# Optimization experiments

Measured on AMD Instinct MI355X. Metric: run time of the kernel, lower is better.

## Reference

```python
import jax, jax.numpy as jnp
import numpy as np
from jax.scipy.special import gammaln

# ---- constants matching init_kwargs ----
D = 64            # num_nodes
K = 64            # DiBS latent rank (k = d default)
P = 32            # n_particles
N_MC = 16         # MC graph samples for score-function grad estimator
PROJ = 128        # proj_dims
N = 2048          # observations
H = 5.0           # h_latent (Frobenius squared-exponential kernel bandwidth)
ALPHA = 0.2       # alpha_linear * t  (single SVGD step)
STEP = 0.005      # SVGD step size
ALPHA_MU = 1.0
ALPHA_LAMBD = float(D + 2)
THETA_MU = 0.0
P_EDGE = 4.0 / (D - 1)          # Erdos-Renyi edge prob (~2 expected edges/node)
LATENT_STD = 1.0 / np.sqrt(K)   # DiBS default latent prior std


def bge_log_marginal(g, data, mu0, alpha_mu, alpha_lambd):
    """BGe log marginal likelihood log p(data | G) for 0/1 adjacency g [d,d]."""
    n, d = data.shape
    small_t = alpha_mu * (alpha_lambd - d - 1.0) / (alpha_mu + 1.0)
    xbar = data.mean(0)
    xc = data - xbar
    R = small_t * jnp.eye(d) + xc.T @ xc \
        + (n * alpha_mu / (n + alpha_mu)) * jnp.outer(xbar - mu0, xbar - mu0)

    def masked_slogdet(mask):  # logdet of R restricted to mask-selected rows/cols
        m = jnp.outer(mask, mask)
        return jnp.linalg.slogdet(m * R + (1.0 - m) * jnp.eye(d))[1]

    def node_score(j):
        parents = g[:, j].astype(R.dtype)
        pj = jnp.maximum(parents, (jnp.arange(d) == j).astype(R.dtype))
        l = jnp.sum(parents)
        log_gamma = (0.5 * (jnp.log(alpha_mu) - jnp.log(n + alpha_mu))
                     + gammaln(0.5 * (n + alpha_lambd - d + l + 1.0))
                     - gammaln(0.5 * (alpha_lambd - d + l + 1.0))
                     - 0.5 * n * jnp.log(jnp.pi)
                     + 0.5 * (alpha_lambd - d + 2.0 * l + 1.0) * jnp.log(small_t))
        return (log_gamma
                + 0.5 * (n + alpha_lambd - d + l) * masked_slogdet(parents)
                - 0.5 * (n + alpha_lambd - d + l + 1.0) * masked_slogdet(pj))

    return jnp.sum(jax.vmap(node_score)(jnp.arange(d)))


def _dense(key, fan_in, fan_out):
    return jax.random.normal(key, (fan_in, fan_out), jnp.float32) * 0.05


def setup_inputs() -> dict:
    key = jax.random.key(0)
    ks = jax.random.split(key, 16)
    return {
        "z_gt": jax.random.normal(ks[0], (N, D), jnp.float32),
        "init_particles_z": jax.random.normal(ks[1], (P, D, K, 2), jnp.float32) * LATENT_STD,
        "enc_w0": _dense(ks[2], D * D, 20), "enc_b0": jnp.zeros(20, jnp.float32),
        "enc_w1": _dense(ks[3], 20, D),     "enc_b1": jnp.zeros(D, jnp.float32),
        "enc_w2": _dense(ks[4], D, D),      "enc_b2": jnp.zeros(D, jnp.float32),
        "mu_w0": _dense(ks[5], D, D), "mu_b0": jnp.zeros(D, jnp.float32),
        "mu_w1": _dense(ks[6], D, D), "mu_b1": jnp.zeros(D, jnp.float32),
        "lv_w0": _dense(ks[7], D, D), "lv_b0": jnp.zeros(D, jnp.float32),
        "lv_w1": _dense(ks[8], D, D), "lv_b1": jnp.zeros(D, jnp.float32),
        "dec_w0": _dense(ks[9], D, 10),       "dec_b0": jnp.zeros(10, jnp.float32),
        "dec_w1": _dense(ks[10], 10, PROJ),   "dec_b1": jnp.zeros(PROJ, jnp.float32),
        "dec_w2": _dense(ks[11], PROJ, PROJ), "dec_b2": jnp.zeros(PROJ, jnp.float32),
        "seed": 0,
    }


def reference(z_gt, init_particles_z, enc_w0, enc_b0, enc_w1, enc_b1, enc_w2, enc_b2,
              mu_w0, mu_b0, mu_w1, mu_b1, lv_w0, lv_b0, lv_w1, lv_b1,
              dec_w0, dec_b0, dec_w1, dec_b1, dec_w2, dec_b2, seed):
    key = jax.random.key(seed)
    d = z_gt.shape[1]
    od = 1.0 - jnp.eye(d)
    z = init_particles_z                                   # [P,d,k,2]
    u, v = z[..., 0], z[..., 1]
    scores = jnp.einsum('pik,pjk->pij', u, v)              # [P,d,d]
    probs = jax.nn.sigmoid(ALPHA * scores) * od            # soft graph, zero diag

    # --- score-function estimate of grad_z log E_G[p(data|G)] (DiBS marginal) ---
    key, sk = jax.random.split(key)
    gs = jax.random.bernoulli(sk, probs[:, None], (P, N_MC, d, d)).astype(z.dtype) * od
    mu0_inf = jnp.zeros(d, z.dtype)
    logp = jax.vmap(jax.vmap(
        lambda g: bge_log_marginal(g, z_gt, mu0_inf, 1.0, d + 2.0)))(gs)   # [P,S]
    w = jax.nn.softmax(logp, axis=1)                       # self-normalized weights
    M = ALPHA * (gs - probs[:, None]) * od                 # d log q(G|Z) / d scores
    grad_u = jnp.einsum('ps,psij,pjk->pik', w, M, v)
    grad_v = jnp.einsum('ps,psij,pik->pjk', w, M, u)

    # --- grad of soft-graph ER prior + Gaussian latent prior ---
    logit_pe = jnp.log(P_EDGE) - jnp.log1p(-P_EDGE)
    Mp = ALPHA * probs * (1.0 - probs) * logit_pe * od
    grad_u = grad_u + jnp.einsum('pij,pjk->pik', Mp, v) - u / (LATENT_STD ** 2)
    grad_v = grad_v + jnp.einsum('pij,pik->pjk', Mp, u) - v / (LATENT_STD ** 2)
    grads = jnp.stack([grad_u, grad_v], axis=-1)           # [P,d,k,2]

    # --- one SVGD step with Frobenius squared-exponential kernel ---
    zf = z.reshape(P, -1)
    gf = grads.reshape(P, -1)
    sq = jnp.sum((zf[:, None] - zf[None]) ** 2, -1)
    Kmat = jnp.exp(-sq / H)                                # symmetric [P,P]
    rep = (-2.0 / H) * (Kmat @ zf - zf * Kmat.sum(1, keepdims=True))
    z_new = z + STEP * ((Kmat @ gf + rep) / P).reshape(z.shape)

    # --- hard graphs: particle_to_g_lim (alpha -> inf) ---
    s2 = jnp.einsum('pik,pjk->pij', z_new[..., 0], z_new[..., 1])
    g_hard = (s2 > 0).astype(z.dtype) * od                 # [P,d,d]

    mu0_bge = jnp.full(d, THETA_MU, z.dtype)
    log_p_z_given_g = jax.vmap(
        lambda g: bge_log_marginal(g, z_gt, mu0_bge, ALPHA_MU, ALPHA_LAMBD))(g_hard)

    # --- q(z | G) encoder (batched over particles) ---
    gf2 = g_hard.reshape(g_hard.shape[0], d * d)
    h = jax.nn.relu(gf2 @ enc_w0 + enc_b0)
    h = jax.nn.relu(h @ enc_w1 + enc_b1)
    h = jax.nn.relu(h @ enc_w2 + enc_b2)
    q_mu = jax.nn.relu(h @ mu_w0 + mu_b0) @ mu_w1 + mu_b1
    q_lv = jax.nn.relu(h @ lv_w0 + lv_b0) @ lv_w1 + lv_b1

    key, rk = jax.random.split(key)
    eps = jax.random.normal(rk, q_lv.shape, q_lv.dtype)
    q_z = q_mu + eps * jnp.exp(0.5 * q_lv)                 # reparameterize

    # --- decoder ---
    hdec = jax.nn.relu(q_z @ dec_w0 + dec_b0)
    hdec = jax.nn.relu(hdec @ dec_w1 + dec_b1)
    recons = hdec @ dec_w2 + dec_b2                        # [P, PROJ]

    return recons, log_p_z_given_g, q_z, q_mu, q_lv, g_hard, z_new
```

## Files before the change

### kernel.cpp

```cpp
#include <hip/hip_runtime.h>
#include <stdint.h>
#include <math.h>

typedef unsigned long long u64;
typedef unsigned int u32;
typedef unsigned short u16;

#define C_P 32
#define C_S 16
#define C_D 64
#define C_N 2048

#define R_OFF      0
#define CTAB_OFF   4160
#define KEYS_OFF   4224
#define PROBS_OFF  4232
#define GROW_OFF   135304
#define GCOL_OFF   168072
#define NS_OFF     200840
#define W_OFF      233608
#define GF_OFF     234120
#define KM_OFF     365192
#define ZN_OFF     365704
#define NS2_OFF    496776

#define WL_LIST0 16

#define HBLK 768
#define TB3 1728
#define TB2 2208
#define TB1 2208
#define TB0 1920
#define E3 (HBLK + TB3)
#define E2 (E3 + TB2)
#define E1 (E2 + TB1)
#define NBLK_ALL (E1 + TB0)

#define O_REC   0
#define O_LOGP  4096
#define O_QZ    4128
#define O_QMU   6176
#define O_QLV   8224
#define O_GH    10272
#define O_ZN    141344
#define O_TOTAL 403488

__device__ __forceinline__ void tf2x32(u32 k0, u32 k1, u32 x0, u32 x1,
                                       u32& o0, u32& o1) {
  u32 ks2 = k0 ^ k1 ^ 0x1BD11BDAu;
  x0 += k0; x1 += k1;
#define TFR(r) { x0 += x1; x1 = (x1 << r) | (x1 >> (32 - r)); x1 ^= x0; }
  TFR(13) TFR(15) TFR(26) TFR(6)   x0 += k1;  x1 += ks2 + 1u;
  TFR(17) TFR(29) TFR(16) TFR(24)  x0 += ks2; x1 += k0 + 2u;
  TFR(13) TFR(15) TFR(26) TFR(6)   x0 += k0;  x1 += k1 + 3u;
  TFR(17) TFR(29) TFR(16) TFR(24)  x0 += k1;  x1 += ks2 + 4u;
  TFR(13) TFR(15) TFR(26) TFR(6)   x0 += ks2; x1 += k0 + 5u;
#undef TFR
  o0 = x0; o1 = x1;
}

__device__ __forceinline__ double d_erfinv(double x) {
  double w = -log1p(-x * x);
  double p;
  if (w < 5.0) {
    w -= 2.5;
    p = 2.81022636e-08;
    p = 3.43273939e-07  + p * w;
    p = -3.5233877e-06  + p * w;
    p = -4.39150654e-06 + p * w;
    p = 0.00021858087   + p * w;
    p = -0.00125372503  + p * w;
    p = -0.00417768164  + p * w;
    p = 0.246640727     + p * w;
    p = 1.50140941      + p * w;
  } else {
    w = sqrt(w) - 3.0;
    p = -0.000200214257;
    p = 0.000100950558  + p * w;
    p = 0.00134934322   + p * w;
    p = -0.00367342844  + p * w;
    p = 0.00573950773   + p * w;
    p = -0.0076224613   + p * w;
    p = 0.00943887047   + p * w;
    p = 1.00167406      + p * w;
    p = 2.83297682      + p * w;
  }
  return p * x;
}

__device__ __forceinline__ double stirl(double z) {
  double zi = 1.0 / z;
  double zi2 = zi * zi;
  double s = (z - 0.5) * log(z) - z + 0.9189385332046727;
  s += zi * (1.0 / 12.0 - zi2 * (1.0 / 360.0 - zi2 * (1.0 / 1260.0)));
  return s;
}

__global__ void k_R(const float* x, double* ws, const int* seedp) {
  __shared__ double pS[8][64], pX[8][64];
  __shared__ double xbar[64];
  int j = blockIdx.x, t = threadIdx.x;
  int i = t & 63, c = t >> 6;
  if (j == 0) {
    if (t < 64) {
      int l = t;
      double term = (l >= 2) ? log((2049.0 + (double)l) / (4.0 * (1.0 + (double)l)))
                             : 0.0;
      double v = term;
#pragma unroll
      for (int off = 2; off <= 32; off <<= 1) {
        double o = __shfl_up(v, off, 64);
        if (l >= off) v += o;
      }
      const double LOG_HALF = -0.6931471805599453;
      double c0 = -0.5 * log(2049.0)
                - 1024.0 * log(3.14159265358979323846);
      double seed = (l & 1)
        ? c0 + stirl(1026.0) + 2.5 * LOG_HALF
        : c0 + stirl(1025.5) + 0.12078223763524522235 + 1.5 * LOG_HALF;
      ws[CTAB_OFF + l] = seed + v;
    }
    if (t < 8) ((u32*)(ws + GF_OFF))[t] = 0;
    if (t == 0) {
      u32 kk0 = 0u, kk1 = (u32)seedp[0];
      u32 a0, a1, s0, s1, r0, r1, d0, d1;
      tf2x32(kk0, kk1, 0u, 0u, a0, a1);
      tf2x32(kk0, kk1, 0u, 1u, s0, s1);
      tf2x32(a0, a1, 0u, 0u, d0, d1); (void)d0; (void)d1;
      tf2x32(a0, a1, 0u, 1u, r0, r1);
      u32* keys = (u32*)(ws + KEYS_OFF);
      keys[0] = s0; keys[1] = s1; keys[2] = r0; keys[3] = r1;
    }
  }
  double sx = 0.0, sxx = 0.0;
  for (int n = c * 256; n < (c + 1) * 256; n++) {
    double xi = (double)x[n * 64 + i];
    double xj = (double)x[n * 64 + j];
    sx += xi; sxx += xi * xj;
  }
  pS[c][i] = sx; pX[c][i] = sxx;
  __syncthreads();
  if (t < 64) {
    double S = 0.0, X = 0.0;
    for (int cc = 0; cc < 8; cc++) { S += pS[cc][i]; X += pX[cc][i]; }
    xbar[i] = S / 2048.0;
    pX[0][i] = X;
  }
  __syncthreads();
  if (t < 64) {
    double xbi = xbar[i], xbj = xbar[j];
    double s = pX[0][i] - 2048.0 * xbi * xbj + (2048.0 / 2049.0) * xbi * xbj;
    if (i == j) s += 0.5;
    ((float*)(ws + R_OFF))[i * 64 + j] = (float)s;
  }
}

__global__ __launch_bounds__(64) void k_probs(const float* z, double* ws) {
  float* probs = (float*)(ws + PROBS_OFF);
  int b = blockIdx.x; int p = b >> 6, i = b & 63;
  int j = threadIdx.x;
  __shared__ float V[64 * 65];
  __shared__ float us[64];
  int k = j;
  us[k] = z[((p * 64 + i) * 64 + k) * 2 + 0];
  for (int jj = 0; jj < 64; jj++)
    V[jj * 65 + k] = z[((p * 64 + jj) * 64 + k) * 2 + 1];
  __syncthreads();
  float s = 0.f;
  for (int kk = 0; kk < 64; kk++)
    s += us[kk] * V[j * 65 + kk];
  float pr = (i == j) ? 0.f : 1.f / (1.f + expf(-0.2f * s));
  probs[(p * 64 + i) * 64 + j] = pr;
}

__global__ void k_sample(double* ws) {
  const float* probs = (const float*)(ws + PROBS_OFF);
  const u32* keys = (const u32*)(ws + KEYS_OFF);
  u64* grow = (u64*)(ws + GROW_OFF);
  u64* gcol = (u64*)(ws + GCOL_OFF);
  u32* wl = (u32*)(ws + GF_OFF);
  int ps = blockIdx.x;
  int p = ps >> 4;
  int j = threadIdx.x;
  u32 k0 = keys[0], k1 = keys[1];
  u64 colmask = 0;
  for (int i = 0; i < 64; i++) {
    u32 lin = (u32)(ps * 4096 + i * 64 + j);
    u32 o0, o1; tf2x32(k0, k1, 0u, lin, o0, o1);
    u32 bits = o0 ^ o1;
    float f = __uint_as_float((bits >> 9) | 0x3f800000u) - 1.0f;
    bool bit = (f < probs[(p * 64 + i) * 64 + j]);
    u64 rm = __ballot(bit);
    if (j == 0) grow[ps * 64 + i] = rm;
    if (bit) colmask |= (1ull << i);
  }
  gcol[ps * 64 + j] = colmask;
  int m = (int)__popcll(colmask) + 1;
  int tier = (m <= 29) ? 0 : (m <= 32) ? 1 : (m <= 35) ? 2 : (m <= 40) ? 3 : 4;
#pragma unroll
  for (int t = 0; t < 5; t++) {
    u64 b = __ballot(tier == t);
    if (tier == t) {
      int leader = (int)__builtin_ctzll(b);
      u32 off = (u32)__popcll(b & ((1ull << j) - 1ull));
      u32 base = 0;
      if (j == leader) base = atomicAdd(&wl[t], (u32)__popcll(b));
      base = (u32)__shfl((int)base, leader, 64);
      wl[WL_LIST0 + t * 32768 + base + off] = (u32)(ps * 64 + j);
    }
  }
}

__device__ __forceinline__ float rdlane(float x, int l) {
  return __uint_as_float(__builtin_amdgcn_readlane(__float_as_uint(x), (u32)l));
}

template<int MMAX>
__device__ __forceinline__ void tier_body(const float* Rf, const double* ctab,
                                          const u64* masks, double* nodescore,
                                          const u32* wl, int tier,
                                          u32 brel, u32 nb, int (*idx)[64]) {
  int w = threadIdx.x >> 6;
  int lane = threadIdx.x & 63;
  u32 cnt = wl[tier];
  const u32* list = wl + WL_LIST0 + tier * 32768;
  for (u32 ti = brel * 4 + (u32)w; ti < cnt; ti += nb * 4) {
    int task = (int)list[ti];
    int j = task & 63;
    u64 mask = masks[task];
    int P = (int)__popcll(mask);
    int m = P + 1;
    idx[w][lane] = 0;
    __builtin_amdgcn_wave_barrier();
    u64 below = mask & ((1ull << lane) - 1ull);
    if ((mask >> lane) & 1ull) idx[w][(int)__popcll(below)] = lane;
    if (lane == 0) idx[w][P] = j;
    __builtin_amdgcn_wave_barrier();
    int myrow = idx[w][lane];
    float v[MMAX];
#pragma unroll
    for (int c = 0; c < MMAX; c++)
      v[c] = Rf[idx[w][c] * 64 + myrow];
    float mypiv = 1.0f;
#pragma unroll
    for (int k = 0; k < MMAX; k++) {
      if (k < m) {
        float dk = rdlane(v[k], k);
        if (lane == k) mypiv = dk;
        float ns = -v[k] * __builtin_amdgcn_rcpf(dk);
#pragma unroll
        for (int b = k + 1; b < MMAX; b++)
          v[b] += ns * rdlane(v[k], b);
      }
    }
    float lastd = __shfl(mypiv, P, 64);
    float lv = (lane < m) ? __logf(mypiv) : 0.f;
    for (int off = 32; off > 0; off >>= 1) lv += __shfl_down(lv, off, 64);
    if (lane == 0) {
      double l = (double)P;
      nodescore[task] = ctab[P]
                      - 0.5 * (2050.0 + l) * (double)__logf(lastd)
                      - 0.5 * (double)lv;
    }
    __builtin_amdgcn_wave_barrier();
  }
}

#define WB() __builtin_amdgcn_wave_barrier()

__device__ void heavy_body(const float* Rf, const double* ctab,
                           const u64* masks, double* nodescore,
                           const u32* wl, u32 brel, u32 nb,
                           float* T, int* idx) {
  if (threadIdx.x >= 64) return;
  int lane = threadIdx.x;
  u32 cnt = wl[4];
  const u32* list = wl + WL_LIST0 + 4 * 32768;
  for (u32 ii = brel; ii < cnt; ii += nb) {
    WB();
    int task = (int)list[ii];
    int j = task & 63;
    u64 mask = masks[task];
    int P = (int)__popcll(mask);
    int m = P + 1;
    u64 below = mask & ((1ull << lane) - 1ull);
    if ((mask >> lane) & 1ull) idx[(int)__popcll(below)] = lane;
    if (lane == 0) idx[P] = j;
    WB();
    int trLane = (lane * (lane + 1)) >> 1;
    if (lane < m) {
      int cidx = idx[lane];
      int tr = 0;
      for (int r = 0; r < m; r++) {
        if (lane <= r) T[tr + lane] = Rf[idx[r] * 64 + cidx];
        tr += r + 1;
      }
    }
    WB();
    float mypiv = 1.0f, lastd = 1.0f;
    float v[40];
#pragma unroll
    for (int c = 0; c < 40; c++)
      v[c] = T[trLane + c];
#pragma unroll
    for (int k = 0; k < 40; k++) {
      if (k < m) {
        float dk = rdlane(v[k], k);
        if (lane == k) mypiv = dk;
        lastd = dk;
        float ns = -v[k] * __builtin_amdgcn_rcpf(dk);
#pragma unroll
        for (int b = k + 1; b < 40; b++)
          v[b] += ns * rdlane(v[k], b);
      }
    }
    if (m > 40) {
      for (int b = 40; b < m; b++) {
        float acc = 0.f;
#pragma unroll
        for (int k = 0; k < 40; k++) {
          float dk = rdlane(v[k], k);
          float abk = rdlane(v[k], b);
          acc += v[k] * abk * __builtin_amdgcn_rcpf(dk);
        }
        if (lane >= b) T[trLane + b] -= acc;
      }
      WB();
      for (int k = 40; k < m; k++) {
        float dk = T[((k * (k + 1)) >> 1) + k];
        if (lane == k) mypiv = dk;
        lastd = dk;
        float sk = T[trLane + k] * __builtin_amdgcn_rcpf(dk);
        for (int b = k + 1; b < m; b++) {
          float abk = T[((b * (b + 1)) >> 1) + k];
          if (lane >= b) T[trLane + b] -= sk * abk;
        }
        WB();
      }
    }
    double vv = (lane < m) ? log((double)mypiv) : 0.0;
    for (int off = 32; off > 0; off >>= 1) vv += __shfl_down(vv, off, 64);
    if (lane == 0) {
      double logB = vv;
      double logA = logB - log((double)lastd);
      double l = (double)P;
      nodescore[task] = ctab[P]
                      + 0.5 * (2050.0 + l) * logA
                      - 0.5 * (2051.0 + l) * logB;
    }
  }
}

__global__ __launch_bounds__(256) void k_chol_all(const float* Rf, const double* ctab,
                                                  const u64* masks, double* nodescore,
                                                  const u32* wl) {
  __shared__ int idx4[4][64];
  __shared__ float T[2080];
  __shared__ int idxh[64];
  u32 b = blockIdx.x;
  if (b < HBLK)    heavy_body(Rf, ctab, masks, nodescore, wl, b, HBLK, T, idxh);
  else if (b < E3) tier_body<40>(Rf, ctab, masks, nodescore, wl, 3, b - HBLK, TB3, idx4);
  else if (b < E2) tier_body<35>(Rf, ctab, masks, nodescore, wl, 2, b - E3, TB2, idx4);
  else if (b < E1) tier_body<32>(Rf, ctab, masks, nodescore, wl, 1, b - E2, TB1, idx4);
  else             tier_body<29>(Rf, ctab, masks, nodescore, wl, 0, b - E1, TB0, idx4);
}

template<bool TRANSPOSE>
__global__ __launch_bounds__(64) void k_chol(const float* Rf, const double* ctab,
                                             const u64* masks, double* nodescore) {
  __shared__ float T[2080];
  __shared__ int idx[64];
  int task = blockIdx.x;
  int j = task & 63;
  int lane = threadIdx.x;
  u64 mask;
  if (TRANSPOSE) {
    int p = task >> 6;
    u64 rm = masks[p * 64 + lane];
    mask = __ballot((rm >> j) & 1ull);
  } else {
    mask = masks[task];
  }
  int P = (int)__popcll(mask);
  int m = P + 1;
  u64 below = mask & ((1ull << lane) - 1ull);
  if ((mask >> lane) & 1ull) idx[(int)__popcll(below)] = lane;
  if (lane == 0) idx[P] = j;
  __syncthreads();
  int trLane = (lane * (lane + 1)) >> 1;
  if (lane < m) {
    int cidx = idx[lane];
    int tr = 0;
    for (int r = 0; r < m; r++) {
      if (lane <= r) T[tr + lane] = Rf[idx[r] * 64 + cidx];
      tr += r + 1;
    }
  }
  __syncthreads();
  float mypiv = 1.0f, lastd = 1.0f;
  float v[40];
#pragma unroll
  for (int c = 0; c < 40; c++)
    v[c] = T[trLane + c];
#pragma unroll
  for (int k = 0; k < 40; k++) {
    if (k < m) {
      float dk = rdlane(v[k], k);
      if (lane == k) mypiv = dk;
      lastd = dk;
      float ns = -v[k] * __builtin_amdgcn_rcpf(dk);
#pragma unroll
      for (int b = k + 1; b < 40; b++)
        v[b] += ns * rdlane(v[k], b);
    }
  }
  if (m > 40) {
    for (int b = 40; b < m; b++) {
      float acc = 0.f;
#pragma unroll
      for (int k = 0; k < 40; k++) {
        float dk = rdlane(v[k], k);
        float abk = rdlane(v[k], b);
        acc += v[k] * abk * __builtin_amdgcn_rcpf(dk);
      }
      if (lane >= b) T[trLane + b] -= acc;
    }
    __syncthreads();
    for (int k = 40; k < m; k++) {
      float dk = T[((k * (k + 1)) >> 1) + k];
      if (lane == k) mypiv = dk;
      lastd = dk;
      float sk = T[trLane + k] * __builtin_amdgcn_rcpf(dk);
      for (int b = k + 1; b < m; b++) {
        float abk = T[((b * (b + 1)) >> 1) + k];
        if (lane >= b) T[trLane + b] -= sk * abk;
      }
      __syncthreads();
    }
  }
  double vv = (lane < m) ? log((double)mypiv) : 0.0;
  for (int off = 32; off > 0; off >>= 1) vv += __shfl_down(vv, off, 64);
  if (lane == 0) {
    double logB = vv;
    double logA = logB - log((double)lastd);
    double l = (double)P;
    nodescore[task] = ctab[P]
                    + 0.5 * (2050.0 + l) * logA
                    - 0.5 * (2051.0 + l) * logB;
  }
}

__global__ void k_logpw(const double* ns, double* w) {
  int p = blockIdx.x, t = threadIdx.x;
  __shared__ double part[64];
  int s = t & 15, c = t >> 4;
  double acc = 0.0;
  for (int j = c * 16; j < (c + 1) * 16; j++)
    acc += ns[(p * 16 + s) * 64 + j];
  part[t] = acc;
  __syncthreads();
  if (t < 16) part[t] = part[t] + part[t + 16] + part[t + 32] + part[t + 48];
  __syncthreads();
  if (t == 0) {
    double m = part[0];
    for (int s2 = 1; s2 < 16; s2++) m = fmax(m, part[s2]);
    double e[16], sum = 0.0;
    for (int s2 = 0; s2 < 16; s2++) { e[s2] = exp(part[s2] - m); sum += e[s2]; }
    for (int s2 = 0; s2 < 16; s2++) w[p * 16 + s2] = e[s2] / sum;
  }
}

__global__ void k_grad(double* ws, const float* z) {
  const float* probs = (const float*)(ws + PROBS_OFF);
  const double* w = ws + W_OFF;
  const u64* grow = (const u64*)(ws + GROW_OFF);
  const u64* gcol = (const u64*)(ws + GCOL_OFF);
  float* gf = (float*)(ws + GF_OFF);
  const float LOGIT = -2.6903717578966254f;
  int bb = blockIdx.x;
  int k = threadIdx.x;
  __shared__ float acc[64];
  if (bb < 2048) {
    int p = bb >> 6, i = bb & 63;
    float gb = 0.f, wsum = 0.f;
    for (int s = 0; s < 16; s++) {
      float wv = (float)w[p * 16 + s];
      wsum += wv;
      gb += wv * (float)((grow[(p * 16 + s) * 64 + i] >> k) & 1ull);
    }
    float pr = probs[(p * 64 + i) * 64 + k];
    float od = (i == k) ? 0.f : 1.f;
    acc[k] = (0.2f * (gb - pr * wsum) + 0.2f * pr * (1.f - pr) * LOGIT) * od;
    __syncthreads();
    float s = 0.f;
    for (int j = 0; j < 64; j++)
      s += acc[j] * z[((p * 64 + j) * 64 + k) * 2 + 1];
    s -= 64.f * z[((p * 64 + i) * 64 + k) * 2 + 0];
    gf[p * 8192 + (i * 64 + k) * 2 + 0] = s;
  } else if (bb < 4096) {
    int b = bb - 2048;
    int p = b >> 6, j = b & 63;
    float gb = 0.f, wsum = 0.f;
    for (int s = 0; s < 16; s++) {
      float wv = (float)w[p * 16 + s];
      wsum += wv;
      gb += wv * (float)((gcol[(p * 16 + s) * 64 + j] >> k) & 1ull);
    }
    float pr = probs[(p * 64 + k) * 64 + j];
    float od = (k == j) ? 0.f : 1.f;
    acc[k] = (0.2f * (gb - pr * wsum) + 0.2f * pr * (1.f - pr) * LOGIT) * od;
    __syncthreads();
    float s = 0.f;
    for (int i = 0; i < 64; i++)
      s += acc[i] * z[((p * 64 + i) * 64 + k) * 2 + 0];
    s -= 64.f * z[((p * 64 + j) * 64 + k) * 2 + 1];
    gf[p * 8192 + (j * 64 + k) * 2 + 1] = s;
  } else {
    float* Km = (float*)(ws + KM_OFF);
    int b = bb - 4096;
    int a = b >> 5, b2 = b & 31;
    float accf = 0.f;
    for (int d0 = k; d0 < 8192; d0 += 64) {
      float diff = z[a * 8192 + d0] - z[b2 * 8192 + d0];
      accf += diff * diff;
    }
    for (int off = 32; off > 0; off >>= 1) accf += __shfl_down(accf, off, 64);
    if (k == 0) Km[a * 32 + b2] = expf(-accf / 5.0f);
  }
}

__global__ void k_znew(const float* z, double* ws, float* out) {
  const float* Km = (const float*)(ws + KM_OFF);
  const float* gf = (const float*)(ws + GF_OFF);
  float* zn = (float*)(ws + ZN_OFF);
  int gid = blockIdx.x * 64 + threadIdx.x;
  int p = gid >> 13, t = gid & 8191;
  float zp = z[p * 8192 + t];
  float accg = 0.f, accz = 0.f, ks = 0.f;
  for (int b = 0; b < 32; b++) {
    float kv = Km[p * 32 + b];
    accg += kv * gf[b * 8192 + t];
    accz += kv * z[b * 8192 + t];
    ks += kv;
  }
  float rep = -0.4f * (accz - zp * ks);
  float v = zp + 0.005f * ((accg + rep) / 32.f);
  zn[p * 8192 + t] = v;
  out[O_ZN + p * 8192 + t] = v;
}

__global__ __launch_bounds__(64) void k_s2col(double* ws, float* out) {
  const float* zn = (const float*)(ws + ZN_OFF);
  u64* grow2 = (u64*)(ws + NS_OFF);
  int b = blockIdx.x; int p = b >> 6, i = b & 63;
  int j = threadIdx.x;
  __shared__ float V[64 * 65];
  __shared__ float us[64];
  int k = j;
  us[k] = zn[p * 8192 + (i * 64 + k) * 2 + 0];
  for (int jj = 0; jj < 64; jj++)
    V[jj * 65 + k] = zn[p * 8192 + (jj * 64 + k) * 2 + 1];
  __syncthreads();
  float s = 0.f;
  for (int kk = 0; kk < 64; kk++)
    s += us[kk] * V[j * 65 + kk];
  bool bit = (i != j) && (s > 0.0f);
  out[O_GH + (p * 64 + i) * 64 + j] = bit ? 1.0f : 0.0f;
  u64 m = __ballot(bit);
  if (j == 0) grow2[p * 64 + i] = m;
}

__global__ __launch_bounds__(256) void k_mlp(double* ws, float* out, const double* ns2,
    const float* ew0, const float* eb0, const float* ew1, const float* eb1,
    const float* ew2, const float* eb2,
    const float* mw0, const float* mb0, const float* mw1, const float* mb1,
    const float* lw0, const float* lb0, const float* lw1, const float* lb1,
    const float* dw0, const float* db0, const float* dw1, const float* db1,
    const float* dw2, const float* db2) {
  int p = blockIdx.x, t = threadIdx.x;
  int w = t >> 6, lane = t & 63;
  const u64* grow2 = (const u64*)(ws + NS_OFF);
  const u32* keys = (const u32*)(ws + KEYS_OFF);
  __shared__ float pt[4][64];
  __shared__ float e0p[4][20];
  __shared__ float h0[20], h1[64], h2[64], hm[64], hl[64];
  __shared__ float qmu[64], qlv[64], qz[64], h3[10], h4[128];

  if (w == 0) {
    double vv = ns2[p * 64 + lane];
    for (int off = 32; off > 0; off >>= 1) vv += __shfl_down(vv, off, 64);
    if (lane == 0) out[O_LOGP + p] = (float)vv;
  }

  {
    int i = t >> 2;
    int jb = (t & 3) * 16;
    u32 m16 = (u32)((grow2[p * 64 + i] >> jb) & 0xFFFFull);
    float acc[20];
#pragma unroll
    for (int o = 0; o < 20; o++) acc[o] = 0.f;
    const float4* wb = (const float4*)(ew0 + (size_t)(t * 16) * 20);
#pragma unroll
    for (int q = 0; q < 16; q++) {
      float mq = (float)((m16 >> q) & 1u);
      float4 r0 = wb[q * 5 + 0], r1 = wb[q * 5 + 1], r2 = wb[q * 5 + 2];
      float4 r3 = wb[q * 5 + 3], r4 = wb[q * 5 + 4];
      acc[0]  += mq * r0.x; acc[1]  += mq * r0.y; acc[2]  += mq * r0.z; acc[3]  += mq * r0.w;
      acc[4]  += mq * r1.x; acc[5]  += mq * r1.y; acc[6]  += mq * r1.z; acc[7]  += mq * r1.w;
      acc[8]  += mq * r2.x; acc[9]  += mq * r2.y; acc[10] += mq * r2.z; acc[11] += mq * r2.w;
      acc[12] += mq * r3.x; acc[13] += mq * r3.y; acc[14] += mq * r3.z; acc[15] += mq * r3.w;
      acc[16] += mq * r4.x; acc[17] += mq * r4.y; acc[18] += mq * r4.z; acc[19] += mq * r4.w;
    }
#pragma unroll
    for (int o = 0; o < 20; o++) {
      float v = acc[o];
      for (int off = 32; off > 0; off >>= 1) v += __shfl_down(v, off, 64);
      if (lane == 0) e0p[w][o] = v;
    }
  }
  __syncthreads();
  if (t < 20)
    h0[t] = fmaxf(eb0[t] + e0p[0][t] + e0p[1][t] + e0p[2][t] + e0p[3][t], 0.f);
  __syncthreads();

  {
    float s = 0.f;
#pragma unroll
    for (int q = 0; q < 5; q++) s += h0[w * 5 + q] * ew1[(w * 5 + q) * 64 + lane];
    pt[w][lane] = s;
  }
  __syncthreads();
  if (w == 0)
    h1[lane] = fmaxf(eb1[lane] + pt[0][lane] + pt[1][lane] + pt[2][lane] + pt[3][lane], 0.f);
  __syncthreads();

  {
    float s = 0.f;
#pragma unroll
    for (int q = 0; q < 16; q++) s += h1[w * 16 + q] * ew2[(w * 16 + q) * 64 + lane];
    pt[w][lane] = s;
  }
  __syncthreads();
  if (w == 0)
    h2[lane] = fmaxf(eb2[lane] + pt[0][lane] + pt[1][lane] + pt[2][lane] + pt[3][lane], 0.f);
  __syncthreads();

  {
    const float* W = (w < 2) ? mw0 : lw0;
    int qb = (w & 1) * 32;
    float s = 0.f;
#pragma unroll
    for (int q = 0; q < 32; q++) s += h2[qb + q] * W[(qb + q) * 64 + lane];
    pt[w][lane] = s;
  }
  __syncthreads();
  if (w == 0) hm[lane] = fmaxf(mb0[lane] + pt[0][lane] + pt[1][lane], 0.f);
  if (w == 1) hl[lane] = fmaxf(lb0[lane] + pt[2][lane] + pt[3][lane], 0.f);
  __syncthreads();

  {
    const float* W = (w < 2) ? mw1 : lw1;
    const float* src = (w < 2) ? hm : hl;
    int qb = (w & 1) * 32;
    float s = 0.f;
#pragma unroll
    for (int q = 0; q < 32; q++) s += src[qb + q] * W[(qb + q) * 64 + lane];
    pt[w][lane] = s;
  }
  __syncthreads();
  if (w == 0) qmu[lane] = mb1[lane] + pt[0][lane] + pt[1][lane];
  if (w == 1) qlv[lane] = lb1[lane] + pt[2][lane] + pt[3][lane];
  __syncthreads();

  if (w == 0) {
    u32 o0, o1;
    tf2x32(keys[2], keys[3], 0u, (u32)(p * 64 + lane), o0, o1);
    u32 bits = o0 ^ o1;
    float f = __uint_as_float((bits >> 9) | 0x3f800000u) - 1.0f;
    float LOF = __uint_as_float(0xBF7FFFFFu);
    float uu = fmaxf(LOF, f * 2.0f + LOF);
    float eps = (float)(1.4142135623730951 * d_erfinv((double)uu));
    float qzv = qmu[lane] + eps * expf(0.5f * qlv[lane]);
    qz[lane] = qzv;
    out[O_QZ  + p * 64 + lane] = qzv;
    out[O_QMU + p * 64 + lane] = qmu[lane];
    out[O_QLV + p * 64 + lane] = qlv[lane];
  }
  __syncthreads();

  {
    float s = 0.f;
    if (lane < 10) {
#pragma unroll
      for (int q = 0; q < 16; q++) s += qz[w * 16 + q] * dw0[(w * 16 + q) * 10 + lane];
    }
    pt[w][lane] = s;
  }
  __syncthreads();
  if (w == 0 && lane < 10)
    h3[lane] = fmaxf(db0[lane] + pt[0][lane] + pt[1][lane] + pt[2][lane] + pt[3][lane], 0.f);
  __syncthreads();

  {
    int o = (w >> 1) * 64 + lane;
    int qb = (w & 1) * 5;
    float s = 0.f;
#pragma unroll
    for (int q = 0; q < 5; q++) s += h3[qb + q] * dw1[(qb + q) * 128 + o];
    pt[w][lane] = s;
  }
  __syncthreads();
  if (w == 0) h4[lane]      = fmaxf(db1[lane]      + pt[0][lane] + pt[1][lane], 0.f);
  if (w == 1) h4[64 + lane] = fmaxf(db1[64 + lane] + pt[2][lane] + pt[3][lane], 0.f);
  __syncthreads();

  {
    int o = (w >> 1) * 64 + lane;
    int qb = (w & 1) * 64;
    float s = 0.f;
#pragma unroll
    for (int q = 0; q < 64; q++) s += h4[qb + q] * dw2[(qb + q) * 128 + o];
    pt[w][lane] = s;
  }
  __syncthreads();
  if (w == 0) out[O_REC + p * 128 + lane]      = db2[lane]      + pt[0][lane] + pt[1][lane];
  if (w == 1) out[O_REC + p * 128 + 64 + lane] = db2[64 + lane] + pt[2][lane] + pt[3][lane];
}

extern "C" void kernel_launch(void* const* d_in, const int* in_sizes, int n_in,
                              void* d_out, int out_size, void* d_ws, size_t ws_size,
                              hipStream_t stream) {
  (void)in_sizes; (void)n_in; (void)out_size; (void)ws_size;
  const float* z_gt = (const float*)d_in[0];
  const float* z0   = (const float*)d_in[1];
  const float* ew0 = (const float*)d_in[2];  const float* eb0 = (const float*)d_in[3];
  const float* ew1 = (const float*)d_in[4];  const float* eb1 = (const float*)d_in[5];
  const float* ew2 = (const float*)d_in[6];  const float* eb2 = (const float*)d_in[7];
  const float* mw0 = (const float*)d_in[8];  const float* mb0 = (const float*)d_in[9];
  const float* mw1 = (const float*)d_in[10]; const float* mb1 = (const float*)d_in[11];
  const float* lw0 = (const float*)d_in[12]; const float* lb0 = (const float*)d_in[13];
  const float* lw1 = (const float*)d_in[14]; const float* lb1 = (const float*)d_in[15];
  const float* dw0 = (const float*)d_in[16]; const float* db0 = (const float*)d_in[17];
  const float* dw1 = (const float*)d_in[18]; const float* db1 = (const float*)d_in[19];
  const float* dw2 = (const float*)d_in[20]; const float* db2 = (const float*)d_in[21];
  const int* seed = (const int*)d_in[22];
  double* ws = (double*)d_ws;
  float* out = (float*)d_out;
  const float* Rf = (const float*)(ws + R_OFF);
  const u32* wl = (const u32*)(ws + GF_OFF);

  k_R<<<64, 512, 0, stream>>>(z_gt, ws, seed);
  k_probs<<<C_P * C_D, 64, 0, stream>>>(z0, ws);
  k_sample<<<C_P * C_S, 64, 0, stream>>>(ws);
  k_chol_all<<<NBLK_ALL, 256, 0, stream>>>(Rf, ws + CTAB_OFF,
      (const u64*)(ws + GCOL_OFF), ws + NS_OFF, wl);
  k_logpw<<<C_P, 64, 0, stream>>>(ws + NS_OFF, ws + W_OFF);
  k_grad<<<2 * C_P * C_D + C_P * C_P, 64, 0, stream>>>(ws, z0);
  k_znew<<<(C_P * 8192) / 64, 64, 0, stream>>>(z0, ws, out);
  k_s2col<<<C_P * C_D, 64, 0, stream>>>(ws, out);
  k_chol<true><<<C_P * C_D, 64, 0, stream>>>(Rf, ws + CTAB_OFF,
      (const u64*)(ws + NS_OFF), ws + NS2_OFF);
  k_mlp<<<C_P, 256, 0, stream>>>(ws, out, ws + NS2_OFF,
      ew0, eb0, ew1, eb1, ew2, eb2,
      mw0, mb0, mw1, mb1, lw0, lb0, lw1, lb1,
      dw0, db0, dw1, db1, dw2, db2);
}
```

Baseline: 350.3 us.

## Pack two small Cholesky tasks per wavefront using half-wave bpermute

Tiers 0 and 1 (masked submatrix size up to 32) are merged into one packed path where each 64-lane wavefront handles two node-score tasks, 32 lanes each. Cross-lane pivot broadcasts use ds_bpermute within each half-wave instead of readlane, and the larger tiers are renumbered with block counts rebalanced. This aims to stop small factorizations from leaving half a wave idle. In exchange, every elimination step now pays a bpermute that goes through the LDS crossbar, and the partner task may be absent when the task count is odd.

```diff
diff --git a/kernel.cpp b/kernel.cpp
--- a/kernel.cpp
+++ b/kernel.cpp
@@ -27,14 +27,13 @@
 #define WL_LIST0 16
 
 #define HBLK 768
-#define TB3 1728
-#define TB2 2208
-#define TB1 2208
-#define TB0 1920
-#define E3 (HBLK + TB3)
-#define E2 (E3 + TB2)
-#define E1 (E2 + TB1)
-#define NBLK_ALL (E1 + TB0)
+#define TB2 1664
+#define TB1 2176
+#define TPK 2048
+#define E_H  (HBLK)
+#define E_2  (E_H + TB2)
+#define E_1  (E_2 + TB1)
+#define NBLK_ALL (E_1 + TPK)
 
 #define O_REC   0
 #define O_LOGP  4096
@@ -196,9 +195,9 @@
   }
   gcol[ps * 64 + j] = colmask;
   int m = (int)__popcll(colmask) + 1;
-  int tier = (m <= 29) ? 0 : (m <= 32) ? 1 : (m <= 35) ? 2 : (m <= 40) ? 3 : 4;
-#pragma unroll
-  for (int t = 0; t < 5; t++) {
+  int tier = (m <= 32) ? 0 : (m <= 35) ? 1 : (m <= 40) ? 2 : 3;
+#pragma unroll
+  for (int t = 0; t < 4; t++) {
     u64 b = __ballot(tier == t);
     if (tier == t) {
       int leader = (int)__builtin_ctzll(b);
@@ -213,6 +212,69 @@
 
 __device__ __forceinline__ float rdlane(float x, int l) {
   return __uint_as_float(__builtin_amdgcn_readlane(__float_as_uint(x), (u32)l));
+}
+
+__device__ __forceinline__ float bperm(int byteaddr, float x) {
+  return __uint_as_float(__builtin_amdgcn_ds_bpermute(byteaddr, __float_as_uint(x)));
+}
+
+__device__ __forceinline__ void packed_body(const float* Rf, const double* ctab,
+                                            const u64* masks, double* nodescore,
+                                            const u32* wl, u32 brel, u32 nb,
+                                            int (*idx)[2][32]) {
+  int w = threadIdx.x >> 6;
+  int lane = threadIdx.x & 63;
+  int half = lane >> 5, l5 = lane & 31;
+  int ab = (lane & 32) << 2;
+  u32 cnt = wl[0];
+  const u32* list = wl + WL_LIST0;
+  u32 npair = (cnt + 1) >> 1;
+  for (u32 ti = brel * 4 + (u32)w; ti < npair; ti += nb * 4) {
+    u32 iA = 2 * ti, iB = iA + 1;
+    bool hasB = (iB < cnt);
+    int task = (int)list[(half && hasB) ? iB : iA];
+    int j = task & 63;
+    u64 mask = masks[task];
+    int P = (int)__popcll(mask);
+    int m = P + 1;
+    idx[w][half][l5] = 0;
+    __builtin_amdgcn_wave_barrier();
+    {
+      u64 below = mask & ((1ull << l5) - 1ull);
+      if ((mask >> l5) & 1ull) idx[w][half][(int)__popcll(below)] = l5;
+      int b2 = l5 + 32;
+      u64 below2 = mask & ((1ull << b2) - 1ull);
+      if ((mask >> b2) & 1ull) idx[w][half][(int)__popcll(below2)] = b2;
+      if (l5 == 0) idx[w][half][P] = j;
+    }
+    __builtin_amdgcn_wave_barrier();
+    int myrow = idx[w][half][l5];
+    float v[32];
+#pragma unroll
+    for (int c = 0; c < 32; c++)
+      v[c] = Rf[idx[w][half][c] * 64 + myrow];
+    float mypiv = 1.0f;
+#pragma unroll
+    for (int k = 0; k < 32; k++) {
+      float dk = bperm(ab + (k << 2), v[k]);
+      mypiv = (l5 == k) ? dk : mypiv;
+      float ns = -v[k] * __builtin_amdgcn_rcpf(dk);
+#pragma unroll
+      for (int b = k + 1; b < 32; b++)
+        v[b] += ns * bperm(ab + (b << 2), v[k]);
+    }
+    float lastd = bperm(ab + (P << 2), mypiv);
+    float lv = (l5 < m) ? __logf(mypiv) : 0.f;
+#pragma unroll
+    for (int off = 16; off > 0; off >>= 1) lv += __shfl_down(lv, off, 32);
+    if (l5 == 0 && (half == 0 || hasB)) {
+      double l = (double)P;
+      nodescore[task] = ctab[P]
+                      - 0.5 * (2050.0 + l) * (double)__logf(lastd)
+                      - 0.5 * (double)lv;
+    }
+    __builtin_amdgcn_wave_barrier();
+  }
 }
 
 template<int MMAX>
@@ -274,8 +336,8 @@
                            float* T, int* idx) {
   if (threadIdx.x >= 64) return;
   int lane = threadIdx.x;
-  u32 cnt = wl[4];
-  const u32* list = wl + WL_LIST0 + 4 * 32768;
+  u32 cnt = wl[3];
+  const u32* list = wl + WL_LIST0 + 3 * 32768;
   for (u32 ii = brel; ii < cnt; ii += nb) {
     WB();
     int task = (int)list[ii];
@@ -355,14 +417,14 @@
                                                   const u64* masks, double* nodescore,
                                                   const u32* wl) {
   __shared__ int idx4[4][64];
+  __shared__ int idxp[4][2][32];
   __shared__ float T[2080];
   __shared__ int idxh[64];
   u32 b = blockIdx.x;
-  if (b < HBLK)    heavy_body(Rf, ctab, masks, nodescore, wl, b, HBLK, T, idxh);
-  else if (b < E3) tier_body<40>(Rf, ctab, masks, nodescore, wl, 3, b - HBLK, TB3, idx4);
-  else if (b < E2) tier_body<35>(Rf, ctab, masks, nodescore, wl, 2, b - E3, TB2, idx4);
-  else if (b < E1) tier_body<32>(Rf, ctab, masks, nodescore, wl, 1, b - E2, TB1, idx4);
-  else             tier_body<29>(Rf, ctab, masks, nodescore, wl, 0, b - E1, TB0, idx4);
+  if (b < E_H)      heavy_body(Rf, ctab, masks, nodescore, wl, b, HBLK, T, idxh);
+  else if (b < E_2) tier_body<40>(Rf, ctab, masks, nodescore, wl, 2, b - E_H, TB2, idx4);
+  else if (b < E_1) tier_body<35>(Rf, ctab, masks, nodescore, wl, 1, b - E_2, TB1, idx4);
+  else              packed_body(Rf, ctab, masks, nodescore, wl, b - E_1, TPK, idxp);
 }
 
 template<bool TRANSPOSE>
```

After: 336.9 us. -3.8%, faster.

## Process two Cholesky tasks per wave in lower tiers and re-tier worklists

Applied to the files above, without the earlier changes.

Adds a tier_body2 variant where each wavefront runs two independent masked Cholesky factorizations at once, interleaving their register-resident elimination steps to raise instruction-level parallelism. Tiers are regrouped from five to four (≤32, ≤36, ≤40, heavy), and block counts per tier are rebalanced. The paired path doubles register arrays, which may raise register pressure or cause spills at MMAX=36, and it pads small tasks up to a larger template size.

```diff
diff --git a/kernel.cpp b/kernel.cpp
--- a/kernel.cpp
+++ b/kernel.cpp
@@ -27,14 +27,13 @@
 #define WL_LIST0 16
 
 #define HBLK 768
-#define TB3 1728
-#define TB2 2208
-#define TB1 2208
-#define TB0 1920
-#define E3 (HBLK + TB3)
-#define E2 (E3 + TB2)
-#define E1 (E2 + TB1)
-#define NBLK_ALL (E1 + TB0)
+#define TB1 1280
+#define TB0 2112
+#define TB2 1312
+#define E_H  (HBLK)
+#define E_1  (E_H + TB1)
+#define E_0  (E_1 + TB0)
+#define NBLK_ALL (E_0 + TB2)
 
 #define O_REC   0
 #define O_LOGP  4096
@@ -196,9 +195,9 @@
   }
   gcol[ps * 64 + j] = colmask;
   int m = (int)__popcll(colmask) + 1;
-  int tier = (m <= 29) ? 0 : (m <= 32) ? 1 : (m <= 35) ? 2 : (m <= 40) ? 3 : 4;
-#pragma unroll
-  for (int t = 0; t < 5; t++) {
+  int tier = (m <= 32) ? 0 : (m <= 36) ? 1 : (m <= 40) ? 2 : 3;
+#pragma unroll
+  for (int t = 0; t < 4; t++) {
     u64 b = __ballot(tier == t);
     if (tier == t) {
       int leader = (int)__builtin_ctzll(b);
@@ -213,6 +212,86 @@
 
 __device__ __forceinline__ float rdlane(float x, int l) {
   return __uint_as_float(__builtin_amdgcn_readlane(__float_as_uint(x), (u32)l));
+}
+
+template<int MMAX>
+__device__ __forceinline__ void tier_body2(const float* Rf, const double* ctab,
+                                           const u64* masks, double* nodescore,
+                                           const u32* wl, int tier,
+                                           u32 brel, u32 nb, int (*idx)[2][64]) {
+  int w = threadIdx.x >> 6;
+  int lane = threadIdx.x & 63;
+  u32 cnt = wl[tier];
+  const u32* list = wl + WL_LIST0 + tier * 32768;
+  u32 npair = (cnt + 1) >> 1;
+  for (u32 ti = brel * 4 + (u32)w; ti < npair; ti += nb * 4) {
+    u32 iA = 2 * ti, iB = iA + 1;
+    bool hasB = (iB < cnt);
+    int taskA = (int)list[iA];
+    int taskB = (int)list[hasB ? iB : iA];
+    u64 maskA = masks[taskA];
+    u64 maskB = masks[taskB];
+    int PA = (int)__popcll(maskA), PB = (int)__popcll(maskB);
+    idx[w][0][lane] = 0;
+    idx[w][1][lane] = 0;
+    __builtin_amdgcn_wave_barrier();
+    {
+      u64 belowA = maskA & ((1ull << lane) - 1ull);
+      if ((maskA >> lane) & 1ull) idx[w][0][(int)__popcll(belowA)] = lane;
+      if (lane == 0) idx[w][0][PA] = taskA & 63;
+      u64 belowB = maskB & ((1ull << lane) - 1ull);
+      if ((maskB >> lane) & 1ull) idx[w][1][(int)__popcll(belowB)] = lane;
+      if (lane == 0) idx[w][1][PB] = taskB & 63;
+    }
+    __builtin_amdgcn_wave_barrier();
+    int rowA = idx[w][0][lane];
+    int rowB = idx[w][1][lane];
+    float va[MMAX], vb[MMAX];
+#pragma unroll
+    for (int c = 0; c < MMAX; c++) {
+      va[c] = Rf[idx[w][0][c] * 64 + rowA];
+      vb[c] = Rf[idx[w][1][c] * 64 + rowB];
+    }
+    float pivA = 1.0f, pivB = 1.0f;
+#pragma unroll
+    for (int k = 0; k < MMAX; k++) {
+      float dkA = rdlane(va[k], k);
+      float dkB = rdlane(vb[k], k);
+      if (lane == k) { pivA = dkA; pivB = dkB; }
+      float nsA = -va[k] * __builtin_amdgcn_rcpf(dkA);
+      float nsB = -vb[k] * __builtin_amdgcn_rcpf(dkB);
+#pragma unroll
+      for (int b2 = k + 1; b2 < MMAX; b2++) {
+        va[b2] += nsA * rdlane(va[k], b2);
+        vb[b2] += nsB * rdlane(vb[k], b2);
+      }
+    }
+    {
+      int mA = PA + 1;
+      float lastd = __shfl(pivA, PA, 64);
+      float lv = (lane < mA) ? __logf(pivA) : 0.f;
+      for (int off = 32; off > 0; off >>= 1) lv += __shfl_down(lv, off, 64);
+      if (lane == 0) {
+        double l = (double)PA;
+        nodescore[taskA] = ctab[PA]
+                         - 0.5 * (2050.0 + l) * (double)__logf(lastd)
+                         - 0.5 * (double)lv;
+      }
+    }
+    if (hasB) {
+      int mB = PB + 1;
+      float lastd = __shfl(pivB, PB, 64);
+      float lv = (lane < mB) ? __logf(pivB) : 0.f;
+      for (int off = 32; off > 0; off >>= 1) lv += __shfl_down(lv, off, 64);
+      if (lane == 0) {
+        double l = (double)PB;
+        nodescore[taskB] = ctab[PB]
+                         - 0.5 * (2050.0 + l) * (double)__logf(lastd)
+                         - 0.5 * (double)lv;
+      }
+    }
+    __builtin_amdgcn_wave_barrier();
+  }
 }
 
 template<int MMAX>
@@ -274,8 +353,8 @@
                            float* T, int* idx) {
   if (threadIdx.x >= 64) return;
   int lane = threadIdx.x;
-  u32 cnt = wl[4];
-  const u32* list = wl + WL_LIST0 + 4 * 32768;
+  u32 cnt = wl[3];
+  const u32* list = wl + WL_LIST0 + 3 * 32768;
   for (u32 ii = brel; ii < cnt; ii += nb) {
     WB();
     int task = (int)list[ii];
@@ -354,15 +433,15 @@
 __global__ __launch_bounds__(256) void k_chol_all(const float* Rf, const double* ctab,
                                                   const u64* masks, double* nodescore,
                                                   const u32* wl) {
+  __shared__ int idx2[4][2][64];
   __shared__ int idx4[4][64];
   __shared__ float T[2080];
   __shared__ int idxh[64];
   u32 b = blockIdx.x;
-  if (b < HBLK)    heavy_body(Rf, ctab, masks, nodescore, wl, b, HBLK, T, idxh);
-  else if (b < E3) tier_body<40>(Rf, ctab, masks, nodescore, wl, 3, b - HBLK, TB3, idx4);
-  else if (b < E2) tier_body<35>(Rf, ctab, masks, nodescore, wl, 2, b - E3, TB2, idx4);
-  else if (b < E1) tier_body<32>(Rf, ctab, masks, nodescore, wl, 1, b - E2, TB1, idx4);
-  else             tier_body<29>(Rf, ctab, masks, nodescore, wl, 0, b - E1, TB0, idx4);
+  if (b < E_H)      heavy_body(Rf, ctab, masks, nodescore, wl, b, HBLK, T, idxh);
+  else if (b < E_1) tier_body2<36>(Rf, ctab, masks, nodescore, wl, 1, b - E_H, TB1, idx2);
+  else if (b < E_0) tier_body2<32>(Rf, ctab, masks, nodescore, wl, 0, b - E_1, TB0, idx2);
+  else              tier_body<40>(Rf, ctab, masks, nodescore, wl, 2, b - E_0, TB2, idx4);
 }
 
 template<bool TRANSPOSE>
```

Measured after the change: 336.5 us. 1.04x faster.
